# Optimization experiments

Hardware: AMD Instinct MI355X
Metric: run time of the kernel (lower is better)

Reference implementation:

```python
import jax, jax.numpy as jnp
import numpy as np

N_NODES = 50000
N_EDGES = 800000
FEAT = 128
HID = 128
CONCAT = 2
OUT_CH = 64
NUM_CL = [[12, 8, 5], [12, 8, 5]]
N_TASKS = 2


def setup_inputs() -> dict:
    key = jax.random.key(0)
    ks = iter(jax.random.split(key, 64))
    s = 0.05

    def w(shape):
        return jax.random.normal(next(ks), shape, dtype=jnp.float32) * s

    inp = {}
    inp["X"] = jax.random.normal(next(ks), (N_TASKS, CONCAT, N_NODES, FEAT), dtype=jnp.float32)
    inp["edge_src"] = jax.random.randint(next(ks), (N_EDGES,), 0, N_NODES, dtype=jnp.int32)
    inp["edge_dst"] = jax.random.randint(next(ks), (N_EDGES,), 0, N_NODES, dtype=jnp.int32)
    inp["y"] = jax.random.randint(next(ks), (N_TASKS, N_NODES, 3), 0, 5, dtype=jnp.int32)

    # LASAGE encoder params (SAGEConv: lin_l (agg, with bias) + lin_r (root, no bias))
    inp["Wl_i0"], inp["bl_i0"], inp["Wr_i0"] = w((FEAT, HID)), w((HID,)), w((FEAT, HID))
    inp["Wl_i1"], inp["bl_i1"], inp["Wr_i1"] = w((FEAT, HID)), w((HID,)), w((FEAT, HID))
    mid = CONCAT * HID  # 256
    inp["Wl_m"], inp["bl_m"], inp["Wr_m"] = w((mid, mid)), w((mid,)), w((mid, mid))
    inp["Wl_o"], inp["bl_o"], inp["Wr_o"] = w((mid, OUT_CH)), w((OUT_CH,)), w((mid, OUT_CH))

    # Task heads, stacked over tasks (same shape per head type across tasks)
    c0, c1, c2 = NUM_CL[0]
    inp["Wl_mt"], inp["bl_mt"], inp["Wr_mt"] = w((N_TASKS, OUT_CH, c0)), w((N_TASKS, c0)), w((N_TASKS, OUT_CH, c0))
    inp["Wl_mt2"], inp["bl_mt2"], inp["Wr_mt2"] = w((N_TASKS, OUT_CH, c1)), w((N_TASKS, c1)), w((N_TASKS, OUT_CH, c1))
    inp["Wl_mt3"], inp["bl_mt3"], inp["Wr_mt3"] = w((N_TASKS, OUT_CH, c2)), w((N_TASKS, c2)), w((N_TASKS, OUT_CH, c2))
    return inp


def reference(X, edge_src, edge_dst, y,
              Wl_i0, bl_i0, Wr_i0, Wl_i1, bl_i1, Wr_i1,
              Wl_m, bl_m, Wr_m, Wl_o, bl_o, Wr_o,
              Wl_mt, bl_mt, Wr_mt, Wl_mt2, bl_mt2, Wr_mt2, Wl_mt3, bl_mt3, Wr_mt3):
    n = X.shape[2]
    deg = jax.ops.segment_sum(jnp.ones_like(edge_dst, dtype=X.dtype), edge_dst, num_segments=n)
    inv_deg = (1.0 / jnp.maximum(deg, 1.0))[:, None]

    def sage(x, Wl, bl, Wr):
        # mean-aggregate neighbor features, then lin_l(agg) + lin_r(x)
        agg = jax.ops.segment_sum(x[edge_src], edge_dst, num_segments=n) * inv_deg
        return agg @ Wl + bl + x @ Wr

    def ce(logits, labels):
        logp = jax.nn.log_softmax(logits, axis=-1)
        return -jnp.mean(jnp.take_along_axis(logp, labels[:, None].astype(jnp.int32), axis=1))

    loss = jnp.float32(0.0)
    for k in range(X.shape[0]):
        # LASAGE encoder (eval mode: dropout inactive)
        h0 = jax.nn.relu(sage(X[k, 0], Wl_i0, bl_i0, Wr_i0))
        h1 = jax.nn.relu(sage(X[k, 1], Wl_i1, bl_i1, Wr_i1))
        xk = jnp.concatenate([h0, h1], axis=-1)  # [N, 256]
        xk = jax.nn.relu(sage(xk, Wl_m, bl_m, Wr_m))
        hk = jax.nn.sigmoid(sage(xk, Wl_o, bl_o, Wr_o))  # [N, 64]
        # per-task heads, sigmoid applied before CE (faithful to source)
        o0 = jax.nn.sigmoid(sage(hk, Wl_mt[k], bl_mt[k], Wr_mt[k]))
        o1 = jax.nn.sigmoid(sage(hk, Wl_mt2[k], bl_mt2[k], Wr_mt2[k]))
        o2 = jax.nn.sigmoid(sage(hk, Wl_mt3[k], bl_mt3[k], Wr_mt3[k]))
        loss = loss + ce(o0, y[k, :, 0]) + ce(o1, y[k, :, 1]) + ce(o2, y[k, :, 2])
    return loss
```

## Files before the change

### kernel.cpp

```cpp
#include <hip/hip_runtime.h>
#include <math.h>

#define NN 50000
#define NE 800000

typedef short bf16x8 __attribute__((ext_vector_type(8)));
typedef float f32x4 __attribute__((ext_vector_type(4)));
typedef float f32x2 __attribute__((ext_vector_type(2)));

__device__ inline ushort f2bf(float f) {
    union { float f; uint u; } v; v.f = f;
    uint r = v.u + 0x7FFFu + ((v.u >> 16) & 1u);
    return (ushort)(r >> 16);
}
__device__ inline float bf2f(ushort h) {
    union { uint u; float f; } v; v.u = ((uint)h) << 16;
    return v.f;
}
__device__ inline uchar f2fp8(float f) {
    float a = fminf(fabsf(f), 448.f);
    union { float f; uint u; } v; v.f = a * 7.52316384526264e-37f;
    uint r = (v.u + 0x7FFFFu + ((v.u >> 20) & 1u)) >> 20;
    if (r > 0x7Eu) r = 0x7Eu;
    union { float f; uint u; } s; s.f = f;
    return (uchar)(r | ((s.u >> 31) << 7));
}
__device__ inline float fp8dec(uint b) {
    union { uint u; float f; } t; t.u = (b & 0x7Fu) << 20;
    union { float f; uint u; } o; o.f = t.f * 1.3292279957849159e36f;
    o.u |= (b & 0x80u) << 24;
    return o.f;
}
__device__ inline void acc_fp8x4(float* acc, uint u) {
#if __has_builtin(__builtin_amdgcn_cvt_pk_f32_fp8)
    f32x2 lo = __builtin_amdgcn_cvt_pk_f32_fp8((int)u, false);
    f32x2 hi = __builtin_amdgcn_cvt_pk_f32_fp8((int)u, true);
    acc[0] += lo[0]; acc[1] += lo[1]; acc[2] += hi[0]; acc[3] += hi[1];
#else
    acc[0] += fp8dec(u & 0xFFu);
    acc[1] += fp8dec((u >> 8) & 0xFFu);
    acc[2] += fp8dec((u >> 16) & 0xFFu);
    acc[3] += fp8dec(u >> 24);
#endif
}
__device__ inline uint pk2bf(float a, float b) {
    return (uint)f2bf(a) | ((uint)f2bf(b) << 16);
}
__device__ inline uint pk4f8(float a, float b, float c, float d) {
    return (uint)f2fp8(a) | ((uint)f2fp8(b) << 8) | ((uint)f2fp8(c) << 16) | ((uint)f2fp8(d) << 24);
}


__global__ void count_edges_k(const int* __restrict__ edst, int* __restrict__ counts, int e) {
    int i = blockIdx.x * blockDim.x + threadIdx.x;
    if (i < e) atomicAdd(&counts[edst[i]], 1);
}

__global__ __launch_bounds__(1024) void scan1_k(const int* __restrict__ counts,
                                                int* __restrict__ row_start,
                                                int* __restrict__ bsum, int n) {
    __shared__ int sd[1024];
    int i = blockIdx.x * 1024 + threadIdx.x;
    int v = (i < n) ? counts[i] : 0;
    sd[threadIdx.x] = v;
    __syncthreads();
    for (int off = 1; off < 1024; off <<= 1) {
        int t = (threadIdx.x >= off) ? sd[threadIdx.x - off] : 0;
        __syncthreads();
        sd[threadIdx.x] += t;
        __syncthreads();
    }
    if (i < n) row_start[i] = sd[threadIdx.x] - v;
    if (threadIdx.x == 1023) bsum[blockIdx.x] = sd[1023];
}

__global__ void scan2_k(int* __restrict__ bsum, int nb) {
    int lane = threadIdx.x;
    int v = (lane < nb) ? bsum[lane] : 0;
    int orig = v;
    for (int off = 1; off < 64; off <<= 1) {
        int t = __shfl_up(v, off);
        if (lane >= off) v += t;
    }
    if (lane < nb) bsum[lane] = v - orig;
}

__global__ void scan3_k(const int* __restrict__ counts, const int* __restrict__ bsum,
                        int* __restrict__ row_start, int* __restrict__ cursor,
                        float* __restrict__ inv_deg, int n, int e) {
    int i = blockIdx.x * blockDim.x + threadIdx.x;
    if (i < n) {
        int rs = row_start[i] + bsum[i >> 10];
        row_start[i] = rs;
        cursor[i] = rs;
        inv_deg[i] = 1.0f / fmaxf((float)counts[i], 1.0f);
        if (i == 0) row_start[n] = e;
    }
}

__global__ void fill_csr_k(const int* __restrict__ esrc, const int* __restrict__ edst,
                           int* __restrict__ cursor, int* __restrict__ csr_src, int e) {
    int i = blockIdx.x * blockDim.x + threadIdx.x;
    if (i < e) {
        int pos = atomicAdd(&cursor[edst[i]], 1);
        csr_src[pos] = esrc[i];
    }
}


struct PrepArg { const float* W1; const float* W2; ushort* Wt; int K; int M; };

__global__ void prep_w4_k(PrepArg p0, PrepArg p1, PrepArg p2, PrepArg p3) {
    PrepArg P = (blockIdx.y == 0) ? p0 : (blockIdx.y == 1) ? p1 : (blockIdx.y == 2) ? p2 : p3;
    int i = blockIdx.x * blockDim.x + threadIdx.x;
    int tot = 2 * P.M * P.K;
    if (i >= tot) return;
    int c = i / P.K, k = i - c * P.K;
    float v = (c < P.M) ? P.W1[(size_t)k * P.M + c] : P.W2[(size_t)k * P.M + (c - P.M)];
    P.Wt[i] = f2bf(v);
}


struct GArg { const void* A; const ushort* Wt; uchar* V8; uchar* R8; };
template<int NY> struct GArgs { GArg a[NY]; };

template<bool A_FP32, int NY>
__global__ __launch_bounds__(256) void gemm_mfma_k(GArgs<NY> P, int K, int M,
                                                   int ldv, int ldr, int n) {
    __shared__ __align__(16) uchar smem[30720];
    const GArg& G = P.a[blockIdx.z];
    const void* __restrict__ Av = G.A;
    const ushort* __restrict__ Wt = G.Wt;

    int tid = threadIdx.x;
    int NC = (2 * M) >> 7; if (NC == 0) NC = 1;
    int cb = blockIdx.x % NC;
    int rb = blockIdx.x / NC;
    int row0 = rb * 64;
    int col0 = cb * 128;
    int lane = tid & 63, wid = tid >> 6;
    int wm = wid & 1, wn = wid >> 1;
    int lrow = lane & 15, lko = (lane >> 4) * 8;

    f32x4 acc[2][4];
    #pragma unroll
    for (int i = 0; i < 2; ++i)
        #pragma unroll
        for (int j = 0; j < 4; ++j)
            acc[i][j] = (f32x4){0.f, 0.f, 0.f, 0.f};

    float4 fA0, fA1;
    uint4 uA, uB0, uB1;

    auto LOAD = [&](int it) {
        int kc = it << 5;
        if constexpr (A_FP32) {
            const float* A = (const float*)Av;
            int r = tid >> 3, s = tid & 7;
            int rg0 = row0 + r, rg1 = rg0 + 32;
            fA0 = (rg0 < n) ? *(const float4*)(A + (size_t)rg0 * K + kc + s * 4)
                            : make_float4(0.f, 0.f, 0.f, 0.f);
            fA1 = (rg1 < n) ? *(const float4*)(A + (size_t)rg1 * K + kc + s * 4)
                            : make_float4(0.f, 0.f, 0.f, 0.f);
        } else {
            const ushort* A = (const ushort*)Av;
            int r = tid >> 2, s = tid & 3;
            int rg = row0 + r;
            uA = (rg < n) ? *(const uint4*)(A + (size_t)rg * K + kc + s * 8)
                          : make_uint4(0u, 0u, 0u, 0u);
        }
        int rB = tid >> 2, sB = tid & 3;
        uB0 = *(const uint4*)(Wt + (size_t)(col0 + rB) * K + kc + sB * 8);
        uB1 = *(const uint4*)(Wt + (size_t)(col0 + rB + 64) * K + kc + sB * 8);
    };
    auto STORE_LDS = [&](int buf) {
        ushort* As = (ushort*)(smem + buf * 15360);
        ushort* Bs = As + 64 * 40;
        if constexpr (A_FP32) {
            int r = tid >> 3, s = tid & 7;
            *(uint2*)(&As[r * 40 + s * 4]) =
                make_uint2(pk2bf(fA0.x, fA0.y), pk2bf(fA0.z, fA0.w));
            *(uint2*)(&As[(r + 32) * 40 + s * 4]) =
                make_uint2(pk2bf(fA1.x, fA1.y), pk2bf(fA1.z, fA1.w));
        } else {
            int r = tid >> 2, s = tid & 3;
            *(uint4*)(&As[r * 40 + s * 8]) = uA;
        }
        int rB = tid >> 2, sB = tid & 3;
        *(uint4*)(&Bs[rB * 40 + sB * 8]) = uB0;
        *(uint4*)(&Bs[(rB + 64) * 40 + sB * 8]) = uB1;
    };

    const int nIt = K >> 5;
    LOAD(0);
    STORE_LDS(0);
    if (nIt > 1) LOAD(1);
    __syncthreads();

    for (int it = 0; it < nIt; ++it) {
        int cur = it & 1;
        if (it + 1 < nIt) STORE_LDS(cur ^ 1);
        if (it + 2 < nIt) LOAD(it + 2);
        {
            const ushort* As = (const ushort*)(smem + cur * 15360);
            const ushort* Bs = As + 64 * 40;
            bf16x8 af[2], bfr[4];
            #pragma unroll
            for (int i = 0; i < 2; ++i)
                af[i] = *(const bf16x8*)(&As[(wm * 32 + i * 16 + lrow) * 40 + lko]);
            #pragma unroll
            for (int j = 0; j < 4; ++j)
                bfr[j] = *(const bf16x8*)(&Bs[(wn * 64 + j * 16 + lrow) * 40 + lko]);
            #pragma unroll
            for (int i = 0; i < 2; ++i)
                #pragma unroll
                for (int j = 0; j < 4; ++j)
                    acc[i][j] = __builtin_amdgcn_mfma_f32_16x16x32_bf16(bfr[j], af[i], acc[i][j], 0, 0, 0);
        }
        __syncthreads();
    }

    uint* C8 = (uint*)smem;
    #pragma unroll
    for (int i = 0; i < 2; ++i) {
        int m = wm * 32 + i * 16 + (lane & 15);
        #pragma unroll
        for (int j = 0; j < 4; ++j) {
            int dc = wn * 16 + j * 4 + (lane >> 4);
            C8[m * 33 + dc] = pk4f8(acc[i][j][0], acc[i][j][1], acc[i][j][2], acc[i][j][3]);
        }
    }
    __syncthreads();
    int row = tid >> 2, seg = tid & 3;
    if (row0 + row < n) {
        uint w[8];
        #pragma unroll
        for (int t = 0; t < 8; ++t) w[t] = C8[row * 33 + seg * 8 + t];
        uchar* base;
        if (M >= 128) {
            base = (col0 < M) ? G.V8 + (size_t)(row0 + row) * ldv + col0 + seg * 32
                              : G.R8 + (size_t)(row0 + row) * ldr + (col0 - M) + seg * 32;
        } else {
            base = (seg < 2) ? G.V8 + (size_t)(row0 + row) * ldv + seg * 32
                             : G.R8 + (size_t)(row0 + row) * ldr + (seg - 2) * 32;
        }
        ((uint4*)base)[0] = make_uint4(w[0], w[1], w[2], w[3]);
        ((uint4*)base)[1] = make_uint4(w[4], w[5], w[6], w[7]);
    }
}


struct Bias4 { const float* b[4]; };

template<int NZ, int U>
__global__ __launch_bounds__(256) void agg_f512_k(const uchar* __restrict__ V8,
                                                  const uchar* __restrict__ R8,
                                                  Bias4 B,
                                                  const float* __restrict__ inv_deg,
                                                  const int* __restrict__ row_start,
                                                  const int* __restrict__ csr_src,
                                                  ushort* __restrict__ xkout,
                                                  size_t tstride, int n) {
    constexpr int LPZ = 64 / NZ;
    int wid  = (blockIdx.x * blockDim.x + threadIdx.x) >> 6;
    int lane = threadIdx.x & 63;
    if (wid >= n) return;
    int dst = wid;
    int c0 = (lane & (LPZ - 1)) * 8;
    const float* bp = B.b[lane / LPZ] + c0;
    int off8 = lane * 8;

    float acc[8];
    #pragma unroll
    for (int q = 0; q < 8; ++q) acc[q] = 0.f;

    int s = row_start[dst], e = row_start[dst + 1];
    for (int g = s; g < e; g += U) {
        int idx[U];
        #pragma unroll
        for (int u = 0; u < U; ++u)
            idx[u] = (g + u < e) ? csr_src[g + u] : -1;
        uint2 d[U];
        #pragma unroll
        for (int u = 0; u < U; ++u) {
            d[u] = make_uint2(0u, 0u);
            if (idx[u] >= 0) d[u] = *(const uint2*)(V8 + (size_t)idx[u] * 512 + off8);
        }
        #pragma unroll
        for (int u = 0; u < U; ++u) {
            acc_fp8x4(acc,     d[u].x);
            acc_fp8x4(acc + 4, d[u].y);
        }
    }

    float inv = inv_deg[dst];
    float r[8];
    #pragma unroll
    for (int q = 0; q < 8; ++q) r[q] = acc[q] * inv + bp[q];
    uint2 rr = *(const uint2*)(R8 + (size_t)dst * 512 + off8);
    acc_fp8x4(r,     rr.x);
    acc_fp8x4(r + 4, rr.y);
    #pragma unroll
    for (int q = 0; q < 8; ++q) r[q] = fmaxf(r[q], 0.f);

    uint4 o;
    o.x = pk2bf(r[0], r[1]); o.y = pk2bf(r[2], r[3]);
    o.z = pk2bf(r[4], r[5]); o.w = pk2bf(r[6], r[7]);
    *(uint4*)(xkout + (size_t)(lane >> 5) * tstride + (size_t)dst * 256 + (lane & 31) * 8) = o;
}


template<int ACT, bool WF8, int U>
__global__ __launch_bounds__(256) void agg_f128_k(const uchar* __restrict__ V8,
                                                  const uchar* __restrict__ R8,
                                                  const float* __restrict__ bias,
                                                  const float* __restrict__ inv_deg,
                                                  const int* __restrict__ row_start,
                                                  const int* __restrict__ csr_src,
                                                  ushort* __restrict__ outb, size_t tstride,
                                                  uchar* __restrict__ out8,
                                                  int n) {
    int wid  = (blockIdx.x * blockDim.x + threadIdx.x) >> 6;
    int lane = threadIdx.x & 63;
    if (wid >= n) return;
    int dst   = wid;
    int sub   = lane & 15;
    int eslot = lane >> 4;
    int task  = sub >> 3;
    int c0    = (sub & 7) * 8;

    float acc[8];
    #pragma unroll
    for (int q = 0; q < 8; ++q) acc[q] = 0.f;

    int s = row_start[dst], e = row_start[dst + 1];
    for (int g = s; g < e; g += 4 * U) {
        int idx[U];
        #pragma unroll
        for (int u = 0; u < U; ++u) {
            int t = g + u * 4 + eslot;
            idx[u] = (t < e) ? csr_src[t] : -1;
        }
        uint2 d[U];
        #pragma unroll
        for (int u = 0; u < U; ++u) {
            d[u] = make_uint2(0u, 0u);
            if (idx[u] >= 0) d[u] = *(const uint2*)(V8 + (size_t)idx[u] * 128 + sub * 8);
        }
        #pragma unroll
        for (int u = 0; u < U; ++u) {
            acc_fp8x4(acc,     d[u].x);
            acc_fp8x4(acc + 4, d[u].y);
        }
    }

    #pragma unroll
    for (int mask = 16; mask < 64; mask <<= 1)
        #pragma unroll
        for (int q = 0; q < 8; ++q)
            acc[q] += __shfl_xor(acc[q], mask);

    if (eslot == 0) {
        float inv = inv_deg[dst];
        float r[8];
        #pragma unroll
        for (int q = 0; q < 8; ++q) r[q] = acc[q] * inv;
        if (bias) {
            #pragma unroll
            for (int q = 0; q < 8; ++q) r[q] += bias[c0 + q];
        }
        if (R8) {
            uint2 rr = *(const uint2*)(R8 + (size_t)dst * 128 + sub * 8);
            acc_fp8x4(r,     rr.x);
            acc_fp8x4(r + 4, rr.y);
        }
        #pragma unroll
        for (int q = 0; q < 8; ++q) {
            if constexpr (ACT == 2) r[q] = 1.f / (1.f + expf(-r[q]));
        }
        uint4 o;
        o.x = pk2bf(r[0], r[1]); o.y = pk2bf(r[2], r[3]);
        o.z = pk2bf(r[4], r[5]); o.w = pk2bf(r[6], r[7]);
        *(uint4*)(outb + (size_t)task * tstride + (size_t)dst * 64 + c0) = o;
        if constexpr (WF8) {
            uint2 o8;
            o8.x = pk4f8(r[0], r[1], r[2], r[3]);
            o8.y = pk4f8(r[4], r[5], r[6], r[7]);
            *(uint2*)(out8 + (size_t)dst * 128 + sub * 8) = o8;
        }
    }
}


template<int C>
__device__ inline float ce_from_z(float* z, int label) {
    float m = -1e30f;
    #pragma unroll
    for (int c = 0; c < C; ++c) { z[c] = 1.f / (1.f + expf(-z[c])); m = fmaxf(m, z[c]); }
    float ssum = 0.f, zl = 0.f;
    #pragma unroll
    for (int c = 0; c < C; ++c) { ssum += expf(z[c] - m); if (c == label) zl = z[c]; }
    return (logf(ssum) + m) - zl;
}

__global__ __launch_bounds__(256) void head_ce_k(const ushort* __restrict__ Ah,
                                                 const ushort* __restrict__ hk,
                                                 const float* __restrict__ Wl1, const float* __restrict__ b1, const float* __restrict__ Wr1,
                                                 const float* __restrict__ Wl2, const float* __restrict__ b2, const float* __restrict__ Wr2,
                                                 const float* __restrict__ Wl3, const float* __restrict__ b3, const float* __restrict__ Wr3,
                                                 const int* __restrict__ yv,
                                                 float* __restrict__ loss_acc, int n) {
    int ty = blockIdx.y;
    int nidx = blockIdx.x * blockDim.x + threadIdx.x;
    Wl1 += ty * 64 * 12; b1 += ty * 12; Wr1 += ty * 64 * 12;
    Wl2 += ty * 64 * 8;  b2 += ty * 8;  Wr2 += ty * 64 * 8;
    Wl3 += ty * 64 * 5;  b3 += ty * 5;  Wr3 += ty * 64 * 5;
    float lsum = 0.f;
    if (nidx < n) {
        float z0[12], z1[8], z2[5];
        #pragma unroll
        for (int c = 0; c < 12; ++c) z0[c] = b1[c];
        #pragma unroll
        for (int c = 0; c < 8; ++c) z1[c] = b2[c];
        #pragma unroll
        for (int c = 0; c < 5; ++c) z2[c] = b3[c];

        const ushort* ap = Ah + ((size_t)ty * NN + nidx) * 64;
        const ushort* hp = hk + ((size_t)ty * NN + nidx) * 64;
        for (int d8 = 0; d8 < 64; d8 += 8) {
            uint4 ua = *(const uint4*)(ap + d8);
            uint4 uh = *(const uint4*)(hp + d8);
            uint aw[4] = {ua.x, ua.y, ua.z, ua.w};
            uint hw[4] = {uh.x, uh.y, uh.z, uh.w};
            #pragma unroll
            for (int p = 0; p < 4; ++p) {
                #pragma unroll
                for (int half = 0; half < 2; ++half) {
                    int d = d8 + p * 2 + half;
                    float av = bf2f((ushort)(half ? (aw[p] >> 16) : (aw[p] & 0xFFFF)));
                    float hv = bf2f((ushort)(half ? (hw[p] >> 16) : (hw[p] & 0xFFFF)));
                    #pragma unroll
                    for (int c = 0; c < 12; ++c)
                        z0[c] = fmaf(av, Wl1[d * 12 + c], fmaf(hv, Wr1[d * 12 + c], z0[c]));
                    #pragma unroll
                    for (int c = 0; c < 8; ++c)
                        z1[c] = fmaf(av, Wl2[d * 8 + c], fmaf(hv, Wr2[d * 8 + c], z1[c]));
                    #pragma unroll
                    for (int c = 0; c < 5; ++c)
                        z2[c] = fmaf(av, Wl3[d * 5 + c], fmaf(hv, Wr3[d * 5 + c], z2[c]));
                }
            }
        }
        const int* yp = yv + ((size_t)ty * NN + nidx) * 3;
        lsum  = ce_from_z<12>(z0, yp[0]);
        lsum += ce_from_z<8 >(z1, yp[1]);
        lsum += ce_from_z<5 >(z2, yp[2]);
    }
    for (int off = 32; off > 0; off >>= 1) lsum += __shfl_down(lsum, off);
    __shared__ float ssum[4];
    int wv = threadIdx.x >> 6, ln = threadIdx.x & 63;
    if (ln == 0) ssum[wv] = lsum;
    __syncthreads();
    if (threadIdx.x == 0) atomicAdd(loss_acc, ssum[0] + ssum[1] + ssum[2] + ssum[3]);
}

__global__ void finalize_k(const float* __restrict__ loss_acc, float* __restrict__ out, int n) {
    out[0] = loss_acc[0] * (1.0f / (float)n);
}


extern "C" void kernel_launch(void* const* d_in, const int* in_sizes, int n_in,
                              void* d_out, int out_size, void* d_ws, size_t ws_size,
                              hipStream_t stream) {
    const float* X    = (const float*)d_in[0];
    const int*   esrc = (const int*)d_in[1];
    const int*   edst = (const int*)d_in[2];
    const int*   y    = (const int*)d_in[3];
    const float* Wl_i[2] = {(const float*)d_in[4], (const float*)d_in[7]};
    const float* bl_i[2] = {(const float*)d_in[5], (const float*)d_in[8]};
    const float* Wr_i[2] = {(const float*)d_in[6], (const float*)d_in[9]};
    const float* Wl_m = (const float*)d_in[10], *bl_m = (const float*)d_in[11], *Wr_m = (const float*)d_in[12];
    const float* Wl_o = (const float*)d_in[13], *bl_o = (const float*)d_in[14], *Wr_o = (const float*)d_in[15];
    const float* Wl_t1 = (const float*)d_in[16], *bl_t1 = (const float*)d_in[17], *Wr_t1 = (const float*)d_in[18];
    const float* Wl_t2 = (const float*)d_in[19], *bl_t2 = (const float*)d_in[20], *Wr_t2 = (const float*)d_in[21];
    const float* Wl_t3 = (const float*)d_in[22], *bl_t3 = (const float*)d_in[23], *Wr_t3 = (const float*)d_in[24];

    const int N = NN, E = NE;
    char* p = (char*)d_ws;
    auto alloc = [&](size_t bytes) -> char* {
        char* r = p;
        p += (bytes + 255) & ~(size_t)255;
        return r;
    };
    int*    counts    = (int*)alloc((size_t)N * 4);
    int*    row_start = (int*)alloc((size_t)(N + 1) * 4);
    int*    cursor    = (int*)alloc((size_t)N * 4);
    int*    bsum      = (int*)alloc(64 * 4);
    int*    csr_src   = (int*)alloc((size_t)E * 4);
    float*  inv_deg   = (float*)alloc((size_t)N * 4);
    float*  loss_acc  = (float*)alloc(256);
    uchar*  V8i  = (uchar*)alloc((size_t)N * 512);
    uchar*  Ri8  = (uchar*)alloc((size_t)N * 512);
    uchar*  V8m  = (uchar*)alloc((size_t)N * 512);
    uchar*  Rm8  = (uchar*)alloc((size_t)N * 512);
    uchar*  V8o  = (uchar*)alloc((size_t)N * 128);
    uchar*  Ro8  = (uchar*)alloc((size_t)N * 128);
    ushort* xk   = (ushort*)alloc((size_t)2 * N * 256 * 2);
    ushort* hk   = (ushort*)alloc((size_t)2 * N * 64 * 2);
    uchar*  hk8  = (uchar*)alloc((size_t)N * 128);
    ushort* Ah   = (ushort*)alloc((size_t)2 * N * 64 * 2);
    ushort* Wt_i0 = (ushort*)alloc((size_t)256 * 128 * 2);
    ushort* Wt_i1 = (ushort*)alloc((size_t)256 * 128 * 2);
    ushort* Wt_m  = (ushort*)alloc((size_t)512 * 256 * 2);
    ushort* Wt_o  = (ushort*)alloc((size_t)128 * 256 * 2);

    hipMemsetAsync(counts, 0, (size_t)N * 4, stream);
    hipMemsetAsync(loss_acc, 0, 4, stream);
    count_edges_k<<<(E + 255) / 256, 256, 0, stream>>>(edst, counts, E);
    const int NB = (N + 1023) / 1024;
    scan1_k<<<NB, 1024, 0, stream>>>(counts, row_start, bsum, N);
    scan2_k<<<1, 64, 0, stream>>>(bsum, NB);
    scan3_k<<<(N + 255) / 256, 256, 0, stream>>>(counts, bsum, row_start, cursor, inv_deg, N, E);
    fill_csr_k<<<(E + 255) / 256, 256, 0, stream>>>(esrc, edst, cursor, csr_src, E);

    {
        PrepArg p0 = {Wl_i[0], Wr_i[0], Wt_i0, 128, 128};
        PrepArg p1 = {Wl_i[1], Wr_i[1], Wt_i1, 128, 128};
        PrepArg p2 = {Wl_m, Wr_m, Wt_m, 256, 256};
        PrepArg p3 = {Wl_o, Wr_o, Wt_o, 256, 64};
        prep_w4_k<<<dim3(512, 4), 256, 0, stream>>>(p0, p1, p2, p3);
    }

    const int RB = (N + 63) / 64;
    const int AGB = (N + 3) / 4;
    const ushort* Wt_i[2] = {Wt_i0, Wt_i1};
    const size_t TSX = (size_t)N * 256;
    const size_t TSH = (size_t)N * 64;

    {
        GArgs<4> P;
        for (int z = 0; z < 4; ++z)
            P.a[z] = {X + (size_t)z * N * 128, Wt_i[z & 1], V8i + z * 128, Ri8 + z * 128};
        gemm_mfma_k<true, 4><<<dim3(RB * 2, 1, 4), 256, 0, stream>>>(P, 128, 128, 512, 512, N);
    }
    {
        Bias4 B = {{bl_i[0], bl_i[1], bl_i[0], bl_i[1]}};
        agg_f512_k<4, 8><<<AGB, 256, 0, stream>>>(V8i, Ri8, B, inv_deg, row_start, csr_src,
                                                  xk, TSX, N);
    }
    {
        GArgs<2> P;
        for (int k = 0; k < 2; ++k)
            P.a[k] = {xk + (size_t)k * TSX, Wt_m, V8m + k * 256, Rm8 + k * 256};
        gemm_mfma_k<false, 2><<<dim3(RB * 4, 1, 2), 256, 0, stream>>>(P, 256, 256, 512, 512, N);
    }
    {
        Bias4 B = {{bl_m, bl_m, nullptr, nullptr}};
        agg_f512_k<2, 8><<<AGB, 256, 0, stream>>>(V8m, Rm8, B, inv_deg, row_start, csr_src,
                                                  xk, TSX, N);
    }
    {
        GArgs<2> P;
        for (int k = 0; k < 2; ++k)
            P.a[k] = {xk + (size_t)k * TSX, Wt_o, V8o + k * 64, Ro8 + k * 64};
        gemm_mfma_k<false, 2><<<dim3(RB, 1, 2), 256, 0, stream>>>(P, 256, 64, 128, 128, N);
    }
    agg_f128_k<2, true, 4><<<AGB, 256, 0, stream>>>(V8o, Ro8, bl_o, inv_deg, row_start, csr_src,
                                                    hk, TSH, hk8, N);
    agg_f128_k<0, false, 4><<<AGB, 256, 0, stream>>>(hk8, nullptr, nullptr, inv_deg, row_start, csr_src,
                                                     Ah, TSH, nullptr, N);
    head_ce_k<<<dim3((N + 255) / 256, 2), 256, 0, stream>>>(Ah, hk,
        Wl_t1, bl_t1, Wr_t1, Wl_t2, bl_t2, Wr_t2, Wl_t3, bl_t3, Wr_t3,
        y, loss_acc, N);

    finalize_k<<<1, 1, 0, stream>>>(loss_acc, (float*)d_out, N);
}
```

Baseline: 465.3 us.

## Use hardware FP8 pack, single-buffer GEMM LDS, and XCD-aware block swizzle

```diff
diff --git a/kernel.cpp b/kernel.cpp
--- a/kernel.cpp
+++ b/kernel.cpp
@@ -17,13 +17,23 @@
     union { uint u; float f; } v; v.u = ((uint)h) << 16;
     return v.f;
 }
-__device__ inline uchar f2fp8(float f) {
+__device__ inline uchar f2fp8_sw(float f) {
     float a = fminf(fabsf(f), 448.f);
     union { float f; uint u; } v; v.f = a * 7.52316384526264e-37f;
     uint r = (v.u + 0x7FFFFu + ((v.u >> 20) & 1u)) >> 20;
     if (r > 0x7Eu) r = 0x7Eu;
     union { float f; uint u; } s; s.f = f;
     return (uchar)(r | ((s.u >> 31) << 7));
+}
+__device__ inline uint pk4f8(float a, float b, float c, float d) {
+#if __has_builtin(__builtin_amdgcn_cvt_pk_fp8_f32)
+    int v = __builtin_amdgcn_cvt_pk_fp8_f32(a, b, 0, false);
+    v = __builtin_amdgcn_cvt_pk_fp8_f32(c, d, v, true);
+    return (uint)v;
+#else
+    return (uint)f2fp8_sw(a) | ((uint)f2fp8_sw(b) << 8) |
+           ((uint)f2fp8_sw(c) << 16) | ((uint)f2fp8_sw(d) << 24);
+#endif
 }
 __device__ inline float fp8dec(uint b) {
     union { uint u; float f; } t; t.u = (b & 0x7Fu) << 20;
@@ -45,9 +55,6 @@
 }
 __device__ inline uint pk2bf(float a, float b) {
     return (uint)f2bf(a) | ((uint)f2bf(b) << 16);
-}
-__device__ inline uint pk4f8(float a, float b, float c, float d) {
-    return (uint)f2fp8(a) | ((uint)f2fp8(b) << 8) | ((uint)f2fp8(c) << 16) | ((uint)f2fp8(d) << 24);
 }
 
 
@@ -127,15 +134,21 @@
 template<bool A_FP32, int NY>
 __global__ __launch_bounds__(256) void gemm_mfma_k(GArgs<NY> P, int K, int M,
                                                    int ldv, int ldr, int n) {
-    __shared__ __align__(16) uchar smem[30720];
+    __shared__ __align__(16) uchar smem[15360];
+    ushort* As = (ushort*)smem;
+    ushort* Bs = As + 64 * 40;
     const GArg& G = P.a[blockIdx.z];
     const void* __restrict__ Av = G.A;
     const ushort* __restrict__ Wt = G.Wt;
 
     int tid = threadIdx.x;
     int NC = (2 * M) >> 7; if (NC == 0) NC = 1;
-    int cb = blockIdx.x % NC;
-    int rb = blockIdx.x / NC;
+    int RBm = (n + 63) >> 6;
+    int xcd = blockIdx.x & 7;
+    int q = blockIdx.x >> 3;
+    int cb = q % NC;
+    int rb = (q / NC) * 8 + xcd;
+    if (rb >= RBm) return;
     int row0 = rb * 64;
     int col0 = cb * 128;
     int lane = tid & 63, wid = tid >> 6;
@@ -173,9 +186,7 @@
         uB0 = *(const uint4*)(Wt + (size_t)(col0 + rB) * K + kc + sB * 8);
         uB1 = *(const uint4*)(Wt + (size_t)(col0 + rB + 64) * K + kc + sB * 8);
     };
-    auto STORE_LDS = [&](int buf) {
-        ushort* As = (ushort*)(smem + buf * 15360);
-        ushort* Bs = As + 64 * 40;
+    auto STORE_LDS = [&]() {
         if constexpr (A_FP32) {
             int r = tid >> 3, s = tid & 7;
             *(uint2*)(&As[r * 40 + s * 4]) =
@@ -193,33 +204,27 @@
 
     const int nIt = K >> 5;
     LOAD(0);
-    STORE_LDS(0);
-    if (nIt > 1) LOAD(1);
-    __syncthreads();
-
     for (int it = 0; it < nIt; ++it) {
-        int cur = it & 1;
-        if (it + 1 < nIt) STORE_LDS(cur ^ 1);
-        if (it + 2 < nIt) LOAD(it + 2);
-        {
-            const ushort* As = (const ushort*)(smem + cur * 15360);
-            const ushort* Bs = As + 64 * 40;
-            bf16x8 af[2], bfr[4];
-            #pragma unroll
-            for (int i = 0; i < 2; ++i)
-                af[i] = *(const bf16x8*)(&As[(wm * 32 + i * 16 + lrow) * 40 + lko]);
+        __syncthreads();
+        STORE_LDS();
+        __syncthreads();
+        if (it + 1 < nIt) LOAD(it + 1);
+
+        bf16x8 af[2], bfr[4];
+        #pragma unroll
+        for (int i = 0; i < 2; ++i)
+            af[i] = *(const bf16x8*)(&As[(wm * 32 + i * 16 + lrow) * 40 + lko]);
+        #pragma unroll
+        for (int j = 0; j < 4; ++j)
+            bfr[j] = *(const bf16x8*)(&Bs[(wn * 64 + j * 16 + lrow) * 40 + lko]);
+        #pragma unroll
+        for (int i = 0; i < 2; ++i)
             #pragma unroll
             for (int j = 0; j < 4; ++j)
-                bfr[j] = *(const bf16x8*)(&Bs[(wn * 64 + j * 16 + lrow) * 40 + lko]);
-            #pragma unroll
-            for (int i = 0; i < 2; ++i)
-                #pragma unroll
-                for (int j = 0; j < 4; ++j)
-                    acc[i][j] = __builtin_amdgcn_mfma_f32_16x16x32_bf16(bfr[j], af[i], acc[i][j], 0, 0, 0);
-        }
-        __syncthreads();
-    }
-
+                acc[i][j] = __builtin_amdgcn_mfma_f32_16x16x32_bf16(bfr[j], af[i], acc[i][j], 0, 0, 0);
+    }
+
+    __syncthreads();
     uint* C8 = (uint*)smem;
     #pragma unroll
     for (int i = 0; i < 2; ++i) {
@@ -531,7 +536,7 @@
         prep_w4_k<<<dim3(512, 4), 256, 0, stream>>>(p0, p1, p2, p3);
     }
 
-    const int RB = (N + 63) / 64;
+    const int RBp = (((N + 63) / 64 + 7) / 8) * 8;
     const int AGB = (N + 3) / 4;
     const ushort* Wt_i[2] = {Wt_i0, Wt_i1};
     const size_t TSX = (size_t)N * 256;
@@ -541,7 +546,7 @@
         GArgs<4> P;
         for (int z = 0; z < 4; ++z)
             P.a[z] = {X + (size_t)z * N * 128, Wt_i[z & 1], V8i + z * 128, Ri8 + z * 128};
-        gemm_mfma_k<true, 4><<<dim3(RB * 2, 1, 4), 256, 0, stream>>>(P, 128, 128, 512, 512, N);
+        gemm_mfma_k<true, 4><<<dim3(RBp * 2, 1, 4), 256, 0, stream>>>(P, 128, 128, 512, 512, N);
     }
     {
         Bias4 B = {{bl_i[0], bl_i[1], bl_i[0], bl_i[1]}};
@@ -552,7 +557,7 @@
         GArgs<2> P;
         for (int k = 0; k < 2; ++k)
             P.a[k] = {xk + (size_t)k * TSX, Wt_m, V8m + k * 256, Rm8 + k * 256};
-        gemm_mfma_k<false, 2><<<dim3(RB * 4, 1, 2), 256, 0, stream>>>(P, 256, 256, 512, 512, N);
+        gemm_mfma_k<false, 2><<<dim3(RBp * 4, 1, 2), 256, 0, stream>>>(P, 256, 256, 512, 512, N);
     }
     {
         Bias4 B = {{bl_m, bl_m, nullptr, nullptr}};
@@ -563,7 +568,7 @@
         GArgs<2> P;
         for (int k = 0; k < 2; ++k)
             P.a[k] = {xk + (size_t)k * TSX, Wt_o, V8o + k * 64, Ro8 + k * 64};
-        gemm_mfma_k<false, 2><<<dim3(RB, 1, 2), 256, 0, stream>>>(P, 256, 64, 128, 128, N);
+        gemm_mfma_k<false, 2><<<dim3(RBp, 1, 2), 256, 0, stream>>>(P, 256, 64, 128, 128, N);
     }
     agg_f128_k<2, true, 4><<<AGB, 256, 0, stream>>>(V8o, Ro8, bl_o, inv_deg, row_start, csr_src,
                                                     hk, TSH, hk8, N);
```

New measurement: 449.7 us. -3.4%, faster.
